# Kernel tuning notes

Hardware: AMD Instinct MI355X
Metric: run time of the kernel (lower is better)

Reference implementation:

```python
import jax, jax.numpy as jnp
import numpy as np

B, X, C = 8, 256, 256  # batch, feature axis, topfreq

def setup_inputs() -> dict:
    key = jax.random.key(0)
    k1, k2, k3, k4 = jax.random.split(key, 4)
    return {
        "amplitude": jax.random.normal(k1, (B, X, C), dtype=jnp.float32),
        "phase": jax.random.normal(k2, (B, X, C), dtype=jnp.float32),
        "A": jax.random.normal(k3, (C, C), dtype=jnp.float32),
        "w_amplitude": jnp.asarray(0.5, dtype=jnp.float32),
        "w_phase": jnp.asarray(0.5, dtype=jnp.float32),
        # uniform noise for gumbel sampling; keep away from 0 to avoid -log(-log(0))
        "gumbel_u": jax.random.uniform(k4, (B, C, C, 2), dtype=jnp.float32, minval=1e-6, maxval=1.0),
    }

def reference(amplitude, phase, A, w_amplitude, w_phase, gumbel_u):
    # pairwise diffs: (b, x, c, c)
    a_diff = amplitude[..., :, None] - amplitude[..., None, :]
    p_diff = phase[..., :, None] - phase[..., None, :]
    fused = w_amplitude * a_diff + w_phase * p_diff
    # einsum 'dd,bxcd->bxcd' == multiply by diag(A) along last dim
    temp = jnp.diagonal(A) * fused
    # einsum 'bxcd,bxcd->bcd' == sum of squares over x
    dist = jnp.sum(temp * temp, axis=1)  # (b, c, c)
    exp_dist = 1.0 / (dist + 1e-10)
    eye = jnp.eye(C, dtype=exp_dist.dtype)
    off_diag = 1.0 - eye
    exp_dist = exp_dist * off_diag
    exp_max = jax.lax.stop_gradient(jnp.max(exp_dist, axis=-1, keepdims=True))
    p = exp_dist / exp_max
    p = (p * off_diag + eye) * 0.99  # (b, c, c) in (0, 0.99]
    # bernoulli via 2-class gumbel-softmax (tau=1, hard, straight-through)
    logit = jnp.log(p / (1.0 - p))
    logits = jnp.stack([logit, -logit], axis=-1)  # (b, c, c, 2)
    g = -jnp.log(-jnp.log(gumbel_u))
    y = jax.nn.softmax(logits + g, axis=-1)
    y0 = y[..., 0]
    hard0 = (y0 > y[..., 1]).astype(y.dtype)
    sample = hard0 - jax.lax.stop_gradient(y0) + y0  # straight-through
    mask = sample.mean(axis=0)  # (c, c)
    return mask
```

## Files before the change

kernel.cpp:

```cpp
#include <hip/hip_runtime.h>

#define BB 8
#define XX 256
#define CC 256
#define TC 4
#define TCE 4
#define NCH 4
#define XCH (XX / NCH)



__device__ __forceinline__ void epilogue(
    float dist0, float dist1, float dist2, float dist3,
    int b, int c0, int d, const float* __restrict__ gu,
    float* __restrict__ out, float (*wmax)[4])
{
    float ed[TCE];
    ed[0] = (d == c0)     ? 0.0f : __fdiv_rn(1.0f, __fadd_rn(dist0, 1e-10f));
    ed[1] = (d == c0 + 1) ? 0.0f : __fdiv_rn(1.0f, __fadd_rn(dist1, 1e-10f));
    ed[2] = (d == c0 + 2) ? 0.0f : __fdiv_rn(1.0f, __fadd_rn(dist2, 1e-10f));
    ed[3] = (d == c0 + 3) ? 0.0f : __fdiv_rn(1.0f, __fadd_rn(dist3, 1e-10f));

    const int wave = threadIdx.x >> 6;
    const int lane = threadIdx.x & 63;
#pragma unroll
    for (int j = 0; j < TCE; ++j) {
        float v = ed[j];
#pragma unroll
        for (int m = 1; m < 64; m <<= 1) v = fmaxf(v, __shfl_xor(v, m));
        if (lane == 0) wmax[j][wave] = v;
    }
    __syncthreads();

#pragma unroll
    for (int j = 0; j < TCE; ++j) {
        const int c = c0 + j;
        float em = fmaxf(fmaxf(wmax[j][0], wmax[j][1]), fmaxf(wmax[j][2], wmax[j][3]));
        float p;
        if (d == c) {
            p = 0.99f;
        } else {
            p = __fmul_rn(__fdiv_rn(ed[j], em), 0.99f);
        }
        float logit = logf(__fdiv_rn(p, __fsub_rn(1.0f, p)));

        const float2 g2 = *(const float2*)(gu + (((size_t)b * CC + c) * CC + d) * 2);
        float g0 = -logf(-logf(g2.x));
        float g1 = -logf(-logf(g2.y));

        float a0 = __fadd_rn(logit, g0);
        float a1 = __fadd_rn(-logit, g1);
        float m  = fmaxf(a0, a1);
        float e0 = expf(__fsub_rn(a0, m));
        float e1 = expf(__fsub_rn(a1, m));
        float s  = __fadd_rn(e0, e1);
        float y0 = __fdiv_rn(e0, s);
        float y1 = __fdiv_rn(e1, s);
        if (y0 > y1) {
            atomicAdd(&out[(size_t)c * CC + d], 0.125f);
        }
    }
}


__global__ __launch_bounds__(256) void k_zero(float* __restrict__ out)
{
    ((float4*)out)[blockIdx.x * 256 + threadIdx.x] = make_float4(0.f, 0.f, 0.f, 0.f);
}


__global__ __launch_bounds__(256) void k_all(
    const float* __restrict__ amp, const float* __restrict__ ph,
    const float* __restrict__ A,   const float* __restrict__ wAp,
    const float* __restrict__ wPp, const float* __restrict__ gu,
    float* __restrict__ out)
{
    const int d  = threadIdx.x;
    const int c0 = blockIdx.x * TC;
    const int b  = blockIdx.y;

    const float wa = wAp[0];
    const float wp = wPp[0];

    __shared__ float uT[XCH * CC];
    __shared__ float sS[CC];
    __shared__ float wmax[TCE][4];

    float w0 = 0.f, w1 = 0.f, w2 = 0.f, w3 = 0.f;

    for (int h = 0; h < NCH; ++h) {
        {
            const float4* aS = (const float4*)(amp + ((size_t)b * XX + h * XCH) * CC);
            const float4* pS = (const float4*)(ph  + ((size_t)b * XX + h * XCH) * CC);
            float4* uT4 = (float4*)uT;
#pragma unroll 8
            for (int k = 0; k < (XCH * CC / 4) / 256; ++k) {
                const int idx = k * 256 + threadIdx.x;
                const float4 a = aS[idx];
                const float4 p = pS[idx];
                float4 u;
                u.x = __fadd_rn(__fmul_rn(wa, a.x), __fmul_rn(wp, p.x));
                u.y = __fadd_rn(__fmul_rn(wa, a.y), __fmul_rn(wp, p.y));
                u.z = __fadd_rn(__fmul_rn(wa, a.z), __fmul_rn(wp, p.z));
                u.w = __fadd_rn(__fmul_rn(wa, a.w), __fmul_rn(wp, p.w));
                uT4[idx] = u;
            }
        }
        __syncthreads();

        float gacc0 = 0.f, gacc1 = 0.f, gacc2 = 0.f, gacc3 = 0.f, sacc = 0.f;
#pragma unroll 4
        for (int x = 0; x < XCH; ++x) {
            const float* row = uT + x * CC;
            const float ud  = row[d];
            const float4 cA = *(const float4*)(row + c0);
            gacc0 = fmaf(cA.x, ud, gacc0);
            gacc1 = fmaf(cA.y, ud, gacc1);
            gacc2 = fmaf(cA.z, ud, gacc2);
            gacc3 = fmaf(cA.w, ud, gacc3);
            sacc  = fmaf(ud, ud, sacc);
        }
        __syncthreads();
        sS[d] = sacc;
        __syncthreads();

        const float t0 = fmaf(-2.0f, gacc0, __fadd_rn(sS[c0 + 0], sacc));
        const float t1 = fmaf(-2.0f, gacc1, __fadd_rn(sS[c0 + 1], sacc));
        const float t2 = fmaf(-2.0f, gacc2, __fadd_rn(sS[c0 + 2], sacc));
        const float t3 = fmaf(-2.0f, gacc3, __fadd_rn(sS[c0 + 3], sacc));
        if (h == 0) {
            w0 = t0; w1 = t1; w2 = t2; w3 = t3;
        } else {
            w0 = __fadd_rn(w0, t0); w1 = __fadd_rn(w1, t1);
            w2 = __fadd_rn(w2, t2); w3 = __fadd_rn(w3, t3);
        }
    }

    const float dAd  = A[(size_t)d * CC + d];
    const float dAd2 = __fmul_rn(dAd, dAd);

    epilogue(__fmul_rn(dAd2, w0), __fmul_rn(dAd2, w1),
             __fmul_rn(dAd2, w2), __fmul_rn(dAd2, w3),
             b, c0, d, gu, out, wmax);
}

extern "C" void kernel_launch(void* const* d_in, const int* in_sizes, int n_in,
                              void* d_out, int out_size, void* d_ws, size_t ws_size,
                              hipStream_t stream) {
    const float* amp = (const float*)d_in[0];
    const float* ph  = (const float*)d_in[1];
    const float* A   = (const float*)d_in[2];
    const float* wa  = (const float*)d_in[3];
    const float* wp  = (const float*)d_in[4];
    const float* gu  = (const float*)d_in[5];
    float* out = (float*)d_out;

    (void)d_ws; (void)ws_size;

    k_zero<<<(CC * CC / 4) / 256, 256, 0, stream>>>(out);
    dim3 g(CC / TC, BB);
    k_all<<<g, 256, 0, stream>>>(amp, ph, A, wa, wp, gu, out);
}
```

Before: 87.08 us.

## Precompute fused u in workspace and stream columns from global memory

Adds a prepass kernel that computes u = wa*amp + wp*ph once into the workspace and also zeroes the output, replacing the separate zero kernel. The main kernel no longer recomputes u per block from both inputs into a large shared tile. It caches only its four c-columns in shared memory and reads each thread's d-column straight from global u, which should be served largely from L2. This removes redundant per-block reading of two inputs and the 64 KB shared staging, which raises occupancy. In exchange it needs a 2 MB workspace and an extra launch, and falls back to the old path if the workspace is too small.

```diff
diff --git a/kernel.cpp b/kernel.cpp
--- a/kernel.cpp
+++ b/kernel.cpp
@@ -63,11 +63,90 @@
 }
 
 
+__global__ __launch_bounds__(256) void k_u(
+    const float* __restrict__ amp, const float* __restrict__ ph,
+    const float* __restrict__ wAp, const float* __restrict__ wPp,
+    float* __restrict__ u, float* __restrict__ out)
+{
+    const float wa = wAp[0], wp = wPp[0];
+    const int i = blockIdx.x * 256 + threadIdx.x;
+    const float4 a = ((const float4*)amp)[i];
+    const float4 p = ((const float4*)ph)[i];
+    float4 r;
+    r.x = __fadd_rn(__fmul_rn(wa, a.x), __fmul_rn(wp, p.x));
+    r.y = __fadd_rn(__fmul_rn(wa, a.y), __fmul_rn(wp, p.y));
+    r.z = __fadd_rn(__fmul_rn(wa, a.z), __fmul_rn(wp, p.z));
+    r.w = __fadd_rn(__fmul_rn(wa, a.w), __fmul_rn(wp, p.w));
+    ((float4*)u)[i] = r;
+
+    if (blockIdx.x < 64) {
+        ((float4*)out)[blockIdx.x * 256 + threadIdx.x] = make_float4(0.f, 0.f, 0.f, 0.f);
+    }
+}
+
+__global__ __launch_bounds__(256) void k_go(
+    const float* __restrict__ u,  const float* __restrict__ A,
+    const float* __restrict__ gu, float* __restrict__ out)
+{
+    const int d  = threadIdx.x;
+    const int c0 = blockIdx.x * TC;
+    const int b  = blockIdx.y;
+
+    __shared__ float4 cols[XX];
+    __shared__ float  sS[CC];
+    __shared__ float  wmax[TCE][4];
+
+    cols[threadIdx.x] =
+        *(const float4*)(u + ((size_t)b * XX + threadIdx.x) * CC + c0);
+    __syncthreads();
+
+    const float* ucol = u + (size_t)b * XX * CC + d;
+
+    float w0 = 0.f, w1 = 0.f, w2 = 0.f, w3 = 0.f;
+
+#pragma unroll
+    for (int h = 0; h < NCH; ++h) {
+        const int x0 = h * XCH;
+        float gacc0 = 0.f, gacc1 = 0.f, gacc2 = 0.f, gacc3 = 0.f, sacc = 0.f;
+#pragma unroll 4
+        for (int x = 0; x < XCH; ++x) {
+            const float ud  = ucol[(size_t)(x0 + x) * CC];
+            const float4 cA = cols[x0 + x];
+            gacc0 = fmaf(cA.x, ud, gacc0);
+            gacc1 = fmaf(cA.y, ud, gacc1);
+            gacc2 = fmaf(cA.z, ud, gacc2);
+            gacc3 = fmaf(cA.w, ud, gacc3);
+            sacc  = fmaf(ud, ud, sacc);
+        }
+        __syncthreads();
+        sS[d] = sacc;
+        __syncthreads();
+
+        const float t0 = fmaf(-2.0f, gacc0, __fadd_rn(sS[c0 + 0], sacc));
+        const float t1 = fmaf(-2.0f, gacc1, __fadd_rn(sS[c0 + 1], sacc));
+        const float t2 = fmaf(-2.0f, gacc2, __fadd_rn(sS[c0 + 2], sacc));
+        const float t3 = fmaf(-2.0f, gacc3, __fadd_rn(sS[c0 + 3], sacc));
+        if (h == 0) {
+            w0 = t0; w1 = t1; w2 = t2; w3 = t3;
+        } else {
+            w0 = __fadd_rn(w0, t0); w1 = __fadd_rn(w1, t1);
+            w2 = __fadd_rn(w2, t2); w3 = __fadd_rn(w3, t3);
+        }
+    }
+
+    const float dAd  = A[(size_t)d * CC + d];
+    const float dAd2 = __fmul_rn(dAd, dAd);
+
+    epilogue(__fmul_rn(dAd2, w0), __fmul_rn(dAd2, w1),
+             __fmul_rn(dAd2, w2), __fmul_rn(dAd2, w3),
+             b, c0, d, gu, out, wmax);
+}
+
+
 __global__ __launch_bounds__(256) void k_zero(float* __restrict__ out)
 {
     ((float4*)out)[blockIdx.x * 256 + threadIdx.x] = make_float4(0.f, 0.f, 0.f, 0.f);
 }
-
 
 __global__ __launch_bounds__(256) void k_all(
     const float* __restrict__ amp, const float* __restrict__ ph,
@@ -98,12 +177,12 @@
                 const int idx = k * 256 + threadIdx.x;
                 const float4 a = aS[idx];
                 const float4 p = pS[idx];
-                float4 u;
-                u.x = __fadd_rn(__fmul_rn(wa, a.x), __fmul_rn(wp, p.x));
-                u.y = __fadd_rn(__fmul_rn(wa, a.y), __fmul_rn(wp, p.y));
-                u.z = __fadd_rn(__fmul_rn(wa, a.z), __fmul_rn(wp, p.z));
-                u.w = __fadd_rn(__fmul_rn(wa, a.w), __fmul_rn(wp, p.w));
-                uT4[idx] = u;
+                float4 uu;
+                uu.x = __fadd_rn(__fmul_rn(wa, a.x), __fmul_rn(wp, p.x));
+                uu.y = __fadd_rn(__fmul_rn(wa, a.y), __fmul_rn(wp, p.y));
+                uu.z = __fadd_rn(__fmul_rn(wa, a.z), __fmul_rn(wp, p.z));
+                uu.w = __fadd_rn(__fmul_rn(wa, a.w), __fmul_rn(wp, p.w));
+                uT4[idx] = uu;
             }
         }
         __syncthreads();
@@ -155,9 +234,15 @@
     const float* gu  = (const float*)d_in[5];
     float* out = (float*)d_out;
 
-    (void)d_ws; (void)ws_size;
-
-    k_zero<<<(CC * CC / 4) / 256, 256, 0, stream>>>(out);
-    dim3 g(CC / TC, BB);
-    k_all<<<g, 256, 0, stream>>>(amp, ph, A, wa, wp, gu, out);
-}
+    const size_t uElems = (size_t)BB * XX * CC;
+    if (ws_size >= uElems * sizeof(float)) {
+        float* ud = (float*)d_ws;
+        k_u<<<(int)(uElems / 4 / 256), 256, 0, stream>>>(amp, ph, wa, wp, ud, out);
+        dim3 g(CC / TC, BB);
+        k_go<<<g, 256, 0, stream>>>(ud, A, gu, out);
+    } else {
+        k_zero<<<(CC * CC / 4) / 256, 256, 0, stream>>>(out);
+        dim3 g(CC / TC, BB);
+        k_all<<<g, 256, 0, stream>>>(amp, ph, A, wa, wp, gu, out);
+    }
+}
```

Result: faster. 84.49 us (-3.0%).
